# Optimization experiments

Measured on AMD Instinct MI355X. Metric: run time of the kernel, lower is better.

Reference implementation:

```python
import jax, jax.numpy as jnp
import numpy as np

D_MODEL = 512
N_HEADS = 16
D_HEAD = D_MODEL // N_HEADS


def _relative_shift(pos_score):
    # pos_score: [B, H, T, T]  (Transformer-XL shift trick)
    B, H, T1, T2 = pos_score.shape
    padded = jnp.pad(pos_score, ((0, 0), (0, 0), (0, 0), (1, 0)))  # [B,H,T1,T2+1]
    padded = padded.reshape(B, H, T2 + 1, T1)
    return padded[:, :, 1:].reshape(B, H, T1, T2)


def setup_inputs() -> dict:
    key = jax.random.key(0)
    ks = jax.random.split(key, 12)
    B, T, D = 4, 1024, D_MODEL
    s = 1.0 / np.sqrt(D)
    return {
        "q": jax.random.normal(ks[0], (B, T, D), jnp.float32),
        "k": jax.random.normal(ks[1], (B, T, D), jnp.float32),
        "v": jax.random.normal(ks[2], (B, T, D), jnp.float32),
        "pos_embedding": jax.random.normal(ks[3], (B, T, D), jnp.float32),
        "Wq": jax.random.normal(ks[4], (D, D), jnp.float32) * s,
        "bq": jnp.zeros((D,), jnp.float32),
        "Wp": jax.random.normal(ks[5], (D, D), jnp.float32) * s,
        "Wf": jax.random.normal(ks[6], (D, D), jnp.float32) * s,
        "bf": jnp.zeros((D,), jnp.float32),
        "u_bias": jax.random.normal(ks[7], (N_HEADS, D_HEAD), jnp.float32) * s,
        "v_bias": jax.random.normal(ks[8], (N_HEADS, D_HEAD), jnp.float32) * s,
    }


def reference(q, k, v, pos_embedding, Wq, bq, Wp, Wf, bf, u_bias, v_bias):
    B, T, D = q.shape
    H, Dh = N_HEADS, D_HEAD
    sqrt_dim = jnp.asarray(np.sqrt(D_MODEL), q.dtype)
    # NOTE: original module uses linear_q for q, k AND v (faithful to source)
    qh = (q @ Wq + bq).reshape(B, T, H, Dh)            # [B,T,H,Dh]
    kh = (k @ Wq + bq).reshape(B, T, H, Dh)
    vh = (v @ Wq + bq).reshape(B, T, H, Dh)
    ph = (pos_embedding @ Wp).reshape(B, T, H, Dh)     # no bias

    content_score = jnp.einsum('bthd,bshd->bhts', qh + u_bias, kh)
    pos_score = jnp.einsum('bthd,bshd->bhts', qh + v_bias, ph)
    pos_score = _relative_shift(pos_score)

    score = (content_score + pos_score) / sqrt_dim     # [B,H,T,T]
    attn = jax.nn.softmax(score, axis=-1)              # dropout identity in eval
    context = jnp.einsum('bhts,bshd->bthd', attn, vh).reshape(B, T, D)
    return context @ Wf + bf
```

## Files before the change

kernel.cpp:

```cpp
#include <hip/hip_runtime.h>
#include <hip/hip_bf16.h>

typedef __bf16 bf16;
typedef bf16 bf16x8 __attribute__((ext_vector_type(8)));
typedef bf16 bf16x4 __attribute__((ext_vector_type(4)));
typedef float f32x4 __attribute__((ext_vector_type(4)));
typedef _Float16 f16x4 __attribute__((ext_vector_type(4)));

#define SCALE_LOG2 0.06376237f


__global__ __launch_bounds__(256) void prep_kernel(
    const float* __restrict__ Wq, const float* __restrict__ Wp, const float* __restrict__ Wf,
    bf16* __restrict__ WqT, bf16* __restrict__ WpT, bf16* __restrict__ WfT)
{
  const int tid = threadIdx.x;
  __shared__ bf16 t[64][72];
  const int m = blockIdx.x >> 6;
  const int tb = blockIdx.x & 63;
  const int tr = tb >> 3, tc = tb & 7;
  const float* W = (m == 0) ? Wq : (m == 1) ? Wp : Wf;
  bf16*        O = (m == 0) ? WqT : (m == 1) ? WpT : WfT;
  const int r = tid >> 2, cg = tid & 3;
  {
    const float* src = W + (size_t)(tr * 64 + r) * 512 + tc * 64 + cg * 16;
    f32x4 a = *(const f32x4*)src, b2 = *(const f32x4*)(src + 4);
    f32x4 c = *(const f32x4*)(src + 8), d = *(const f32x4*)(src + 12);
    bf16x8 lo, hi;
#pragma unroll
    for (int j = 0; j < 4; j++) { lo[j] = (bf16)a[j]; lo[4 + j] = (bf16)b2[j]; hi[j] = (bf16)c[j]; hi[4 + j] = (bf16)d[j]; }
    *(bf16x8*)(&t[r][cg * 16])     = lo;
    *(bf16x8*)(&t[r][cg * 16 + 8]) = hi;
  }
  __syncthreads();
  bf16x8 o0, o1;
#pragma unroll
  for (int j = 0; j < 8; j++) { o0[j] = t[cg * 16 + j][r]; o1[j] = t[cg * 16 + 8 + j][r]; }
  bf16* dst = O + (size_t)(tc * 64 + r) * 512 + tr * 64 + cg * 16;
  *(bf16x8*)dst = o0;
  *(bf16x8*)(dst + 8) = o1;
}

__global__ __launch_bounds__(256) void proj_gemm(
    const float* __restrict__ q, const float* __restrict__ k, const float* __restrict__ v,
    const float* __restrict__ pos,
    const bf16* __restrict__ WqT, const bf16* __restrict__ WpT, const float* __restrict__ bq,
    bf16* __restrict__ qh, bf16* __restrict__ kh, bf16* __restrict__ vT, bf16* __restrict__ phx)
{
  __shared__ bf16 As[128 * 72];
  __shared__ bf16 Bs[128 * 72];
  const int tid = threadIdx.x;
  const int wave = tid >> 6, lane = tid & 63, quad = lane >> 4, ln = lane & 15;
  const int wg = blockIdx.x;
  const int xcd = wg & 7, sidx = wg >> 3;
  const int tn = sidx & 3;
  const int tm = xcd + ((sidx >> 2) << 3);
  const int kind = tm >> 5;
  const int rr0 = (tm & 31) * 128;
  const float* X = (kind == 0) ? q : (kind == 1) ? k : (kind == 2) ? v : pos;
  const bf16* WT = ((kind < 3) ? WqT : WpT) + (size_t)tn * 128 * 512;
  const int qn_ = (wave & 1) * 64;
  const int qr_ = (wave >> 1) * 64;
  const int srow = tid >> 2, scg = tid & 3;

  f32x4 acc[4][4] = {};

  for (int kk = 0; kk < 8; kk++) {
    const int k0 = kk * 64;
    {
      const float* p0 = X + (size_t)(rr0 + srow) * 512 + k0 + scg * 16;
      const float* p1 = X + (size_t)(rr0 + srow + 64) * 512 + k0 + scg * 16;
#pragma unroll
      for (int h = 0; h < 2; h++) {
        const float* p = h ? p1 : p0;
        f32x4 a = *(const f32x4*)p, b2 = *(const f32x4*)(p + 4);
        f32x4 c = *(const f32x4*)(p + 8), d = *(const f32x4*)(p + 12);
        bf16x8 lo, hi;
#pragma unroll
        for (int j = 0; j < 4; j++) { lo[j] = (bf16)a[j]; lo[4 + j] = (bf16)b2[j]; hi[j] = (bf16)c[j]; hi[4 + j] = (bf16)d[j]; }
        *(bf16x8*)(As + (srow + h * 64) * 72 + scg * 16)     = lo;
        *(bf16x8*)(As + (srow + h * 64) * 72 + scg * 16 + 8) = hi;
      }
      const bf16* w0 = WT + (size_t)srow * 512 + k0 + scg * 16;
      const bf16* w1 = WT + (size_t)(srow + 64) * 512 + k0 + scg * 16;
      *(bf16x8*)(Bs + srow * 72 + scg * 16)            = *(const bf16x8*)w0;
      *(bf16x8*)(Bs + srow * 72 + scg * 16 + 8)        = *(const bf16x8*)(w0 + 8);
      *(bf16x8*)(Bs + (srow + 64) * 72 + scg * 16)     = *(const bf16x8*)w1;
      *(bf16x8*)(Bs + (srow + 64) * 72 + scg * 16 + 8) = *(const bf16x8*)(w1 + 8);
    }
    __syncthreads();
#pragma unroll
    for (int ks = 0; ks < 2; ks++) {
      bf16x8 wf[4], xf[4];
#pragma unroll
      for (int i = 0; i < 4; i++) {
        wf[i] = *(const bf16x8*)(Bs + (qn_ + i * 16 + ln) * 72 + ks * 32 + quad * 8);
        xf[i] = *(const bf16x8*)(As + (qr_ + i * 16 + ln) * 72 + ks * 32 + quad * 8);
      }
#pragma unroll
      for (int i = 0; i < 4; i++)
#pragma unroll
        for (int j = 0; j < 4; j++)
          acc[i][j] = __builtin_amdgcn_mfma_f32_16x16x32_bf16(wf[i], xf[j], acc[i][j], 0, 0, 0);
    }
    __syncthreads();
  }

#pragma unroll
  for (int i = 0; i < 4; i++) {
    const int nn0 = tn * 128 + qn_ + i * 16 + quad * 4;
    const int dd0 = nn0 & 31, hh = nn0 >> 5;
    f32x4 b4 = {0.f, 0.f, 0.f, 0.f};
    if (kind < 3) b4 = *(const f32x4*)(bq + nn0);
#pragma unroll
    for (int j = 0; j < 4; j++) {
      const int rr = rr0 + qr_ + j * 16 + ln;
      const int bb = rr >> 10, tt = rr & 1023;
      const size_t base = (size_t)(bb * 16 + hh);
      bf16x4 pk;
#pragma unroll
      for (int r = 0; r < 4; r++) pk[r] = (bf16)(acc[i][j][r] + b4[r]);
      if (kind == 0)      *(bf16x4*)(qh + (base * 1024 + tt) * 32 + dd0) = pk;
      else if (kind == 1) *(bf16x4*)(kh + (base * 1024 + tt) * 32 + dd0) = pk;
      else if (kind == 2) {
#pragma unroll
        for (int r = 0; r < 4; r++) vT[(base * 32 + dd0 + r) * 1024 + tt] = pk[r];
      } else {
        *(bf16x4*)(phx + (base * 2048 + tt) * 32 + dd0) = pk;
        if (tt <= 1021) *(bf16x4*)(phx + (base * 2048 + tt + 1025) * 32 + dd0) = pk;
        if (tt == 1023) {
          bf16x4 zz = {};
          *(bf16x4*)(phx + (base * 2048 + 1024) * 32 + dd0) = zz;
          *(bf16x4*)(phx + (base * 2048 + 2047) * 32 + dd0) = zz;
        }
      }
    }
  }
}

__global__ __launch_bounds__(256, 4) void attn_kernel(
    const bf16* __restrict__ qh, const bf16* __restrict__ kh,
    const bf16* __restrict__ vT, const bf16* __restrict__ phx,
    const float* __restrict__ u_bias, const float* __restrict__ v_bias,
    float* __restrict__ Oa, float* __restrict__ Ob,
    float* __restrict__ la, float* __restrict__ lb)
{
  __shared__ bf16     kst[64 * 40];
  __shared__ bf16     phs[128 * 40];
  __shared__ bf16     vst[32 * 72];
  __shared__ _Float16 fs[4 * 16 * 84];
  __shared__ bf16     pb[4 * 16 * 72];

  const int tid = threadIdx.x;
  const int wave = tid >> 6, lane = tid & 63, quad = lane >> 4, ln = lane & 15;
  const int wg = blockIdx.x;
  const int bh = wg & 63;
  const int rest = wg >> 6;
  const int tq = rest & 15, sc = rest >> 4;
  const int h = bh & 15, b = bh >> 4;
  const int t0 = tq * 64;
  const bf16* qh_h  = qh  + (size_t)bh * 1024 * 32;
  const bf16* kh_h  = kh  + (size_t)bh * 1024 * 32;
  const bf16* vT_h  = vT  + (size_t)bh * 32 * 1024;
  const bf16* phx_h = phx + (size_t)bh * 2048 * 32;

  _Float16* fsw = fs + wave * 16 * 84;
  bf16*     pbw = pb + wave * 16 * 72;

  const int sr4 = tid >> 2, sc4 = tid & 3;
  const int sr8 = tid >> 3, sc8 = tid & 7;

  bf16x8 qu, qva, qvn;
  {
    const int t = t0 + wave * 16 + ln;
    bf16x8 q0 = *(const bf16x8*)(qh_h + (size_t)t * 32 + quad * 8);
    bf16x8 q1 = *(const bf16x8*)(qh_h + (size_t)(t + 1) * 32 + quad * 8);
    const float* ubp = u_bias + h * 32 + quad * 8;
    const float* vbp = v_bias + h * 32 + quad * 8;
#pragma unroll
    for (int j = 0; j < 8; j++) {
      qu[j]  = (bf16)(((float)q0[j] + ubp[j]) * SCALE_LOG2);
      qva[j] = (bf16)(((float)q0[j] + vbp[j]) * SCALE_LOG2);
      qvn[j] = (bf16)(((float)q1[j] + vbp[j]) * SCALE_LOG2);
    }
  }

  f32x4 O0 = {0.f, 0.f, 0.f, 0.f}, O1 = {0.f, 0.f, 0.f, 0.f};
  float l_lane = 0.0f;
  const f32x4 zf = {0.f, 0.f, 0.f, 0.f};

  const int si0 = sc * 8;

  bf16x8 g0, g1, g2, g3;
  {
    const int s0p = si0 * 64, jbp = s0p - t0 + 960;
    g0 = *(const bf16x8*)(kh_h  + (size_t)(s0p + sr4) * 32 + sc4 * 8);
    g1 = *(const bf16x8*)(phx_h + (size_t)(jbp + sr4) * 32 + sc4 * 8);
    g2 = *(const bf16x8*)(phx_h + (size_t)(jbp + 64 + sr4) * 32 + sc4 * 8);
    g3 = *(const bf16x8*)(vT_h  + (size_t)sr8 * 1024 + s0p + sc8 * 8);
  }

  for (int si = si0; si < si0 + 8; si++) {
    const int s0 = si * 64;
    const int jbase = s0 - t0 + 960;
    const int jb0 = jbase + (3 - wave) * 16;

    __syncthreads();

    *(bf16x8*)(kst + sr4 * 40 + sc4 * 8)        = g0;
    *(bf16x8*)(phs + sr4 * 40 + sc4 * 8)        = g1;
    *(bf16x8*)(phs + (64 + sr4) * 40 + sc4 * 8) = g2;
    *(bf16x8*)(vst + sr8 * 72 + sc8 * 8)        = g3;

    __syncthreads();

    if (si != si0 + 7) {
      const int s0n = s0 + 64, jbn = jbase + 64;
      g0 = *(const bf16x8*)(kh_h  + (size_t)(s0n + sr4) * 32 + sc4 * 8);
      g1 = *(const bf16x8*)(phx_h + (size_t)(jbn + sr4) * 32 + sc4 * 8);
      g2 = *(const bf16x8*)(phx_h + (size_t)(jbn + 64 + sr4) * 32 + sc4 * 8);
      g3 = *(const bf16x8*)(vT_h  + (size_t)sr8 * 1024 + s0n + sc8 * 8);
    }

#pragma unroll
    for (int i = 0; i < 5; i++) {
      const int row = (3 - wave + i) * 16 + ln;
      bf16x8 pbf = *(const bf16x8*)(phs + row * 40 + quad * 8);
      bf16x8 bsel = (jb0 + i * 16 >= 1024) ? qvn : qva;
      f32x4 f = __builtin_amdgcn_mfma_f32_16x16x32_bf16(pbf, bsel, zf, 0, 0, 0);
      f16x4 fh;
#pragma unroll
      for (int r = 0; r < 4; r++) fh[r] = (_Float16)f[r];
      *(f16x4*)(fsw + ln * 84 + i * 16 + quad * 4) = fh;
    }

    f32x4 c[4];
#pragma unroll
    for (int cs = 0; cs < 4; cs++) {
      bf16x8 kbf = *(const bf16x8*)(kst + (cs * 16 + ln) * 40 + quad * 8);
      c[cs] = __builtin_amdgcn_mfma_f32_16x16x32_bf16(kbf, qu, zf, 0, 0, 0);
    }

#pragma unroll
    for (int cs = 0; cs < 4; cs++) {
      bf16x4 pk;
#pragma unroll
      for (int r = 0; r < 4; r++) {
        const int col = cs * 16 + quad * 4 + r - ln + 15;
        const float p = __builtin_amdgcn_exp2f(c[cs][r] + (float)fsw[ln * 84 + col]);
        l_lane += p;
        pk[r] = (bf16)p;
      }
      *(bf16x4*)(pbw + ln * 72 + cs * 16 + quad * 4) = pk;
    }

#pragma unroll
    for (int kb = 0; kb < 2; kb++) {
      bf16x8 a  = *(const bf16x8*)(pbw + ln * 72 + kb * 32 + quad * 8);
      bf16x8 b0 = *(const bf16x8*)(vst + ln * 72 + kb * 32 + quad * 8);
      bf16x8 b1 = *(const bf16x8*)(vst + (16 + ln) * 72 + kb * 32 + quad * 8);
      O0 = __builtin_amdgcn_mfma_f32_16x16x32_bf16(a, b0, O0, 0, 0, 0);
      O1 = __builtin_amdgcn_mfma_f32_16x16x32_bf16(a, b1, O1, 0, 0, 0);
    }
  }

  l_lane += __shfl_xor(l_lane, 16);
  l_lane += __shfl_xor(l_lane, 32);

  float* Op = sc ? Ob : Oa;
  float* lp = sc ? lb : la;
#pragma unroll
  for (int r = 0; r < 4; r++) {
    const int t = t0 + wave * 16 + quad * 4 + r;
    const size_t o = ((size_t)(b * 1024 + t)) * 512 + h * 32;
    Op[o + ln]      = O0[r];
    Op[o + 16 + ln] = O1[r];
  }
  if (lane < 16) lp[(size_t)bh * 1024 + t0 + wave * 16 + lane] = l_lane;
}

__global__ __launch_bounds__(256) void out_gemm(
    const float* __restrict__ Oa, const float* __restrict__ Ob,
    const float* __restrict__ la, const float* __restrict__ lb,
    const bf16* __restrict__ WfT, const float* __restrict__ bfv,
    float* __restrict__ out)
{
  __shared__ bf16 As[64 * 40];
  __shared__ bf16 Bs[128 * 40];
  __shared__ float linv[16 * 64];
  const int tid = threadIdx.x;
  const int wave = tid >> 6, lane = tid & 63, quad = lane >> 4, ln = lane & 15;
  const int wg = blockIdx.x;
  const int xcd = wg & 7, sidx = wg >> 3;
  const int tn = sidx & 3;
  const int tm = xcd + ((sidx >> 2) << 3);
  const int rr0 = tm * 64;
  const bf16* WT = WfT + (size_t)tn * 128 * 512;
  const int qm = (wave & 1) * 32, qn = (wave >> 1) * 64;
  const int srow = tid >> 2, scg = tid & 3;

  for (int e = tid; e < 1024; e += 256) {
    const int hh = e >> 6, r = e & 63;
    const int row = rr0 + r;
    const int b_ = row >> 10, t_ = row & 1023;
    const size_t li = ((size_t)(b_ * 16 + hh)) * 1024 + t_;
    linv[e] = 1.0f / (la[li] + lb[li]);
  }
  __syncthreads();

  f32x4 acc[2][4] = {};
  for (int kk = 0; kk < 16; kk++) {
    const int k0 = kk * 32;
    {
      const float* pa = Oa + (size_t)(rr0 + srow) * 512 + k0 + scg * 8;
      const float* pcb = Ob + (size_t)(rr0 + srow) * 512 + k0 + scg * 8;
      f32x4 a0 = *(const f32x4*)pa,  a1 = *(const f32x4*)(pa + 4);
      f32x4 c0 = *(const f32x4*)pcb, c1 = *(const f32x4*)(pcb + 4);
      const float s = linv[kk * 64 + srow];
      bf16x8 t8;
#pragma unroll
      for (int j = 0; j < 4; j++) {
        t8[j]     = (bf16)((a0[j] + c0[j]) * s);
        t8[4 + j] = (bf16)((a1[j] + c1[j]) * s);
      }
      *(bf16x8*)(As + srow * 40 + scg * 8) = t8;
    }
    *(bf16x8*)(Bs + srow * 40 + scg * 8)        = *(const bf16x8*)(WT + (size_t)srow * 512 + k0 + scg * 8);
    *(bf16x8*)(Bs + (srow + 64) * 40 + scg * 8) = *(const bf16x8*)(WT + (size_t)(srow + 64) * 512 + k0 + scg * 8);
    __syncthreads();
    bf16x8 af[2], bfm[4];
#pragma unroll
    for (int i = 0; i < 2; i++)
      af[i] = *(const bf16x8*)(As + (qm + i * 16 + ln) * 40 + quad * 8);
#pragma unroll
    for (int j = 0; j < 4; j++)
      bfm[j] = *(const bf16x8*)(Bs + (qn + j * 16 + ln) * 40 + quad * 8);
#pragma unroll
    for (int i = 0; i < 2; i++)
#pragma unroll
      for (int j = 0; j < 4; j++)
        acc[i][j] = __builtin_amdgcn_mfma_f32_16x16x32_bf16(af[i], bfm[j], acc[i][j], 0, 0, 0);
    __syncthreads();
  }

#pragma unroll
  for (int i = 0; i < 2; i++)
#pragma unroll
    for (int j = 0; j < 4; j++) {
      const int nn = tn * 128 + qn + j * 16 + ln;
      const float bias = bfv[nn];
#pragma unroll
      for (int r = 0; r < 4; r++) {
        const int rr = rr0 + qm + i * 16 + quad * 4 + r;
        out[(size_t)rr * 512 + nn] = acc[i][j][r] + bias;
      }
    }
}

extern "C" void kernel_launch(void* const* d_in, const int* in_sizes, int n_in,
                              void* d_out, int out_size, void* d_ws, size_t ws_size,
                              hipStream_t stream) {
  const float* q   = (const float*)d_in[0];
  const float* k   = (const float*)d_in[1];
  const float* v   = (const float*)d_in[2];
  const float* pe  = (const float*)d_in[3];
  const float* Wq  = (const float*)d_in[4];
  const float* bq  = (const float*)d_in[5];
  const float* Wp  = (const float*)d_in[6];
  const float* Wf  = (const float*)d_in[7];
  const float* bfv = (const float*)d_in[8];
  const float* ub  = (const float*)d_in[9];
  const float* vb  = (const float*)d_in[10];

  bf16* ws  = (bf16*)d_ws;
  bf16* qh  = ws;
  bf16* kh  = qh + 2097152;
  bf16* vT  = kh + 2097152;
  bf16* phx = vT + 2097152;
  bf16* WqT = phx + 4194304;
  bf16* WpT = WqT + 262144;
  bf16* WfT = WpT + 262144;
  float* Oa = (float*)(WfT + 262144);
  float* Ob = Oa + 2097152;
  float* la = Ob + 2097152;
  float* lb = la + 65536;

  prep_kernel<<<192, 256, 0, stream>>>(Wq, Wp, Wf, WqT, WpT, WfT);
  proj_gemm<<<512, 256, 0, stream>>>(q, k, v, pe, WqT, WpT, bq, qh, kh, vT, phx);
  attn_kernel<<<2048, 256, 0, stream>>>(qh, kh, vT, phx, ub, vb, Oa, Ob, la, lb);
  out_gemm<<<256, 256, 0, stream>>>(Oa, Ob, la, lb, WfT, bfv, (float*)d_out);
}
```

Before: 183.5 us.

## Prefetch GEMM tiles into registers, stage V transpose via LDS, vectorize shift gather

In the projection and output GEMMs, the next K-slice of global data is now loaded into registers while the current slice is multiplied. This hides global load latency behind the MFMAs at the cost of more registers. The V projection epilogue now transposes through a padded LDS tile, so vT gets coalesced 16-byte stores instead of scattered 2-byte stores, which adds shared memory. In the attention kernel, the per-element relative-shift gather from LDS becomes two 64-bit loads plus a funnel shift.

After: 162.0 us. 11.7% less time.

```diff
diff --git a/kernel.cpp b/kernel.cpp
--- a/kernel.cpp
+++ b/kernel.cpp
@@ -49,6 +49,7 @@
 {
   __shared__ bf16 As[128 * 72];
   __shared__ bf16 Bs[128 * 72];
+  __shared__ bf16 vtile[128 * 132];
   const int tid = threadIdx.x;
   const int wave = tid >> 6, lane = tid & 63, quad = lane >> 4, ln = lane & 15;
   const int wg = blockIdx.x;
@@ -65,30 +66,52 @@
 
   f32x4 acc[4][4] = {};
 
+  f32x4  xa0[4], xa1[4];
+  bf16x8 wr0[2], wr1[2];
+  {
+    const float* p0 = X + (size_t)(rr0 + srow) * 512 + scg * 16;
+    const float* p1 = X + (size_t)(rr0 + srow + 64) * 512 + scg * 16;
+#pragma unroll
+    for (int u = 0; u < 4; u++) { xa0[u] = *(const f32x4*)(p0 + u * 4); xa1[u] = *(const f32x4*)(p1 + u * 4); }
+    const bf16* w0 = WT + (size_t)srow * 512 + scg * 16;
+    const bf16* w1 = WT + (size_t)(srow + 64) * 512 + scg * 16;
+    wr0[0] = *(const bf16x8*)w0; wr0[1] = *(const bf16x8*)(w0 + 8);
+    wr1[0] = *(const bf16x8*)w1; wr1[1] = *(const bf16x8*)(w1 + 8);
+  }
+
   for (int kk = 0; kk < 8; kk++) {
-    const int k0 = kk * 64;
+    __syncthreads();
     {
-      const float* p0 = X + (size_t)(rr0 + srow) * 512 + k0 + scg * 16;
-      const float* p1 = X + (size_t)(rr0 + srow + 64) * 512 + k0 + scg * 16;
-#pragma unroll
-      for (int h = 0; h < 2; h++) {
-        const float* p = h ? p1 : p0;
-        f32x4 a = *(const f32x4*)p, b2 = *(const f32x4*)(p + 4);
-        f32x4 c = *(const f32x4*)(p + 8), d = *(const f32x4*)(p + 12);
-        bf16x8 lo, hi;
-#pragma unroll
-        for (int j = 0; j < 4; j++) { lo[j] = (bf16)a[j]; lo[4 + j] = (bf16)b2[j]; hi[j] = (bf16)c[j]; hi[4 + j] = (bf16)d[j]; }
-        *(bf16x8*)(As + (srow + h * 64) * 72 + scg * 16)     = lo;
-        *(bf16x8*)(As + (srow + h * 64) * 72 + scg * 16 + 8) = hi;
-      }
-      const bf16* w0 = WT + (size_t)srow * 512 + k0 + scg * 16;
-      const bf16* w1 = WT + (size_t)(srow + 64) * 512 + k0 + scg * 16;
-      *(bf16x8*)(Bs + srow * 72 + scg * 16)            = *(const bf16x8*)w0;
-      *(bf16x8*)(Bs + srow * 72 + scg * 16 + 8)        = *(const bf16x8*)(w0 + 8);
-      *(bf16x8*)(Bs + (srow + 64) * 72 + scg * 16)     = *(const bf16x8*)w1;
-      *(bf16x8*)(Bs + (srow + 64) * 72 + scg * 16 + 8) = *(const bf16x8*)(w1 + 8);
-    }
-    __syncthreads();
+      bf16x8 lo, hi;
+#pragma unroll
+      for (int j = 0; j < 4; j++) { lo[j] = (bf16)xa0[j >> 2 ? 0 : 0][0], lo[j] = (bf16)xa0[0][j]; }
+#pragma unroll
+      for (int j = 0; j < 4; j++) { lo[j] = (bf16)xa0[0][j]; lo[4 + j] = (bf16)xa0[1][j]; hi[j] = (bf16)xa0[2][j]; hi[4 + j] = (bf16)xa0[3][j]; }
+      *(bf16x8*)(As + srow * 72 + scg * 16)     = lo;
+      *(bf16x8*)(As + srow * 72 + scg * 16 + 8) = hi;
+#pragma unroll
+      for (int j = 0; j < 4; j++) { lo[j] = (bf16)xa1[0][j]; lo[4 + j] = (bf16)xa1[1][j]; hi[j] = (bf16)xa1[2][j]; hi[4 + j] = (bf16)xa1[3][j]; }
+      *(bf16x8*)(As + (srow + 64) * 72 + scg * 16)     = lo;
+      *(bf16x8*)(As + (srow + 64) * 72 + scg * 16 + 8) = hi;
+      *(bf16x8*)(Bs + srow * 72 + scg * 16)            = wr0[0];
+      *(bf16x8*)(Bs + srow * 72 + scg * 16 + 8)        = wr0[1];
+      *(bf16x8*)(Bs + (srow + 64) * 72 + scg * 16)     = wr1[0];
+      *(bf16x8*)(Bs + (srow + 64) * 72 + scg * 16 + 8) = wr1[1];
+    }
+    __syncthreads();
+
+    if (kk < 7) {
+      const int k0n = (kk + 1) * 64;
+      const float* p0 = X + (size_t)(rr0 + srow) * 512 + k0n + scg * 16;
+      const float* p1 = X + (size_t)(rr0 + srow + 64) * 512 + k0n + scg * 16;
+#pragma unroll
+      for (int u = 0; u < 4; u++) { xa0[u] = *(const f32x4*)(p0 + u * 4); xa1[u] = *(const f32x4*)(p1 + u * 4); }
+      const bf16* w0 = WT + (size_t)srow * 512 + k0n + scg * 16;
+      const bf16* w1 = WT + (size_t)(srow + 64) * 512 + k0n + scg * 16;
+      wr0[0] = *(const bf16x8*)w0; wr0[1] = *(const bf16x8*)(w0 + 8);
+      wr1[0] = *(const bf16x8*)w1; wr1[1] = *(const bf16x8*)(w1 + 8);
+    }
+
 #pragma unroll
     for (int ks = 0; ks < 2; ks++) {
       bf16x8 wf[4], xf[4];
@@ -103,35 +126,59 @@
         for (int j = 0; j < 4; j++)
           acc[i][j] = __builtin_amdgcn_mfma_f32_16x16x32_bf16(wf[i], xf[j], acc[i][j], 0, 0, 0);
     }
-    __syncthreads();
-  }
-
-#pragma unroll
-  for (int i = 0; i < 4; i++) {
-    const int nn0 = tn * 128 + qn_ + i * 16 + quad * 4;
-    const int dd0 = nn0 & 31, hh = nn0 >> 5;
-    f32x4 b4 = {0.f, 0.f, 0.f, 0.f};
-    if (kind < 3) b4 = *(const f32x4*)(bq + nn0);
-#pragma unroll
-    for (int j = 0; j < 4; j++) {
-      const int rr = rr0 + qr_ + j * 16 + ln;
-      const int bb = rr >> 10, tt = rr & 1023;
-      const size_t base = (size_t)(bb * 16 + hh);
-      bf16x4 pk;
-#pragma unroll
-      for (int r = 0; r < 4; r++) pk[r] = (bf16)(acc[i][j][r] + b4[r]);
-      if (kind == 0)      *(bf16x4*)(qh + (base * 1024 + tt) * 32 + dd0) = pk;
-      else if (kind == 1) *(bf16x4*)(kh + (base * 1024 + tt) * 32 + dd0) = pk;
-      else if (kind == 2) {
-#pragma unroll
-        for (int r = 0; r < 4; r++) vT[(base * 32 + dd0 + r) * 1024 + tt] = pk[r];
-      } else {
-        *(bf16x4*)(phx + (base * 2048 + tt) * 32 + dd0) = pk;
-        if (tt <= 1021) *(bf16x4*)(phx + (base * 2048 + tt + 1025) * 32 + dd0) = pk;
-        if (tt == 1023) {
-          bf16x4 zz = {};
-          *(bf16x4*)(phx + (base * 2048 + 1024) * 32 + dd0) = zz;
-          *(bf16x4*)(phx + (base * 2048 + 2047) * 32 + dd0) = zz;
+  }
+  __syncthreads();
+
+  if (kind == 2) {
+#pragma unroll
+    for (int i = 0; i < 4; i++) {
+      const int nloc = qn_ + i * 16 + quad * 4;
+      f32x4 b4 = *(const f32x4*)(bq + tn * 128 + nloc);
+#pragma unroll
+      for (int j = 0; j < 4; j++) {
+        const int mloc = qr_ + j * 16 + ln;
+        bf16x4 pk;
+#pragma unroll
+        for (int r = 0; r < 4; r++) pk[r] = (bf16)(acc[i][j][r] + b4[r]);
+        *(bf16x4*)(vtile + mloc * 132 + nloc) = pk;
+      }
+    }
+    __syncthreads();
+    const int n = tid >> 1, mh = (tid & 1) * 64;
+    const int bb2 = rr0 >> 10, tt0 = rr0 & 1023;
+    bf16* vdst = vT + ((size_t)(bb2 * 16 + tn * 4 + (n >> 5)) * 32 + (n & 31)) * 1024 + tt0 + mh;
+#pragma unroll
+    for (int c = 0; c < 8; c++) {
+      bf16x8 oc;
+#pragma unroll
+      for (int e = 0; e < 8; e++) oc[e] = vtile[(mh + c * 8 + e) * 132 + n];
+      *(bf16x8*)(vdst + c * 8) = oc;
+    }
+  } else {
+#pragma unroll
+    for (int i = 0; i < 4; i++) {
+      const int nn0 = tn * 128 + qn_ + i * 16 + quad * 4;
+      const int dd0 = nn0 & 31, hh = nn0 >> 5;
+      f32x4 b4 = {0.f, 0.f, 0.f, 0.f};
+      if (kind < 3) b4 = *(const f32x4*)(bq + nn0);
+#pragma unroll
+      for (int j = 0; j < 4; j++) {
+        const int rr = rr0 + qr_ + j * 16 + ln;
+        const int bb = rr >> 10, tt = rr & 1023;
+        const size_t base = (size_t)(bb * 16 + hh);
+        bf16x4 pk;
+#pragma unroll
+        for (int r = 0; r < 4; r++) pk[r] = (bf16)(acc[i][j][r] + b4[r]);
+        if (kind == 0)      *(bf16x4*)(qh + (base * 1024 + tt) * 32 + dd0) = pk;
+        else if (kind == 1) *(bf16x4*)(kh + (base * 1024 + tt) * 32 + dd0) = pk;
+        else {
+          *(bf16x4*)(phx + (base * 2048 + tt) * 32 + dd0) = pk;
+          if (tt <= 1021) *(bf16x4*)(phx + (base * 2048 + tt + 1025) * 32 + dd0) = pk;
+          if (tt == 1023) {
+            bf16x4 zz = {};
+            *(bf16x4*)(phx + (base * 2048 + 1024) * 32 + dd0) = zz;
+            *(bf16x4*)(phx + (base * 2048 + 2047) * 32 + dd0) = zz;
+          }
         }
       }
     }
@@ -170,6 +217,9 @@
   const int sr4 = tid >> 2, sc4 = tid & 3;
   const int sr8 = tid >> 3, sc8 = tid & 7;
 
+  const int Ab  = quad * 4 + ((15 - ln) & ~3);
+  const int msh = ((15 - ln) & 3) * 16;
+
   bf16x8 qu, qva, qvn;
   {
     const int t = t0 + wave * 16 + ln;
@@ -241,13 +291,17 @@
       c[cs] = __builtin_amdgcn_mfma_f32_16x16x32_bf16(kbf, qu, zf, 0, 0, 0);
     }
 
+    const _Float16* rowp = fsw + ln * 84;
 #pragma unroll
     for (int cs = 0; cs < 4; cs++) {
+      const uint64_t v0 = *(const uint64_t*)(rowp + cs * 16 + Ab);
+      const uint64_t v1 = *(const uint64_t*)(rowp + cs * 16 + Ab + 4);
+      union { uint64_t u; f16x4 v; } W;
+      W.u = (v0 >> msh) | ((v1 << 1) << (63 - msh));
       bf16x4 pk;
 #pragma unroll
       for (int r = 0; r < 4; r++) {
-        const int col = cs * 16 + quad * 4 + r - ln + 15;
-        const float p = __builtin_amdgcn_exp2f(c[cs][r] + (float)fsw[ln * 84 + col]);
+        const float p = __builtin_amdgcn_exp2f(c[cs][r] + (float)W.v[r]);
         l_lane += p;
         pk[r] = (bf16)p;
       }
@@ -299,6 +353,17 @@
   const int qm = (wave & 1) * 32, qn = (wave >> 1) * 64;
   const int srow = tid >> 2, scg = tid & 3;
 
+  f32x4 a0, a1, c0, c1;
+  bf16x8 b0r, b1r;
+  {
+    const float* pa  = Oa + (size_t)(rr0 + srow) * 512 + scg * 8;
+    const float* pcb = Ob + (size_t)(rr0 + srow) * 512 + scg * 8;
+    a0 = *(const f32x4*)pa;  a1 = *(const f32x4*)(pa + 4);
+    c0 = *(const f32x4*)pcb; c1 = *(const f32x4*)(pcb + 4);
+    b0r = *(const bf16x8*)(WT + (size_t)srow * 512 + scg * 8);
+    b1r = *(const bf16x8*)(WT + (size_t)(srow + 64) * 512 + scg * 8);
+  }
+
   for (int e = tid; e < 1024; e += 256) {
     const int hh = e >> 6, r = e & 63;
     const int row = rr0 + r;
@@ -306,16 +371,11 @@
     const size_t li = ((size_t)(b_ * 16 + hh)) * 1024 + t_;
     linv[e] = 1.0f / (la[li] + lb[li]);
   }
-  __syncthreads();
 
   f32x4 acc[2][4] = {};
   for (int kk = 0; kk < 16; kk++) {
-    const int k0 = kk * 32;
+    __syncthreads();
     {
-      const float* pa = Oa + (size_t)(rr0 + srow) * 512 + k0 + scg * 8;
-      const float* pcb = Ob + (size_t)(rr0 + srow) * 512 + k0 + scg * 8;
-      f32x4 a0 = *(const f32x4*)pa,  a1 = *(const f32x4*)(pa + 4);
-      f32x4 c0 = *(const f32x4*)pcb, c1 = *(const f32x4*)(pcb + 4);
       const float s = linv[kk * 64 + srow];
       bf16x8 t8;
 #pragma unroll
@@ -323,11 +383,22 @@
         t8[j]     = (bf16)((a0[j] + c0[j]) * s);
         t8[4 + j] = (bf16)((a1[j] + c1[j]) * s);
       }
-      *(bf16x8*)(As + srow * 40 + scg * 8) = t8;
-    }
-    *(bf16x8*)(Bs + srow * 40 + scg * 8)        = *(const bf16x8*)(WT + (size_t)srow * 512 + k0 + scg * 8);
-    *(bf16x8*)(Bs + (srow + 64) * 40 + scg * 8) = *(const bf16x8*)(WT + (size_t)(srow + 64) * 512 + k0 + scg * 8);
-    __syncthreads();
+      *(bf16x8*)(As + srow * 40 + scg * 8)        = t8;
+      *(bf16x8*)(Bs + srow * 40 + scg * 8)        = b0r;
+      *(bf16x8*)(Bs + (srow + 64) * 40 + scg * 8) = b1r;
+    }
+    __syncthreads();
+
+    if (kk < 15) {
+      const int k0n = (kk + 1) * 32;
+      const float* pa  = Oa + (size_t)(rr0 + srow) * 512 + k0n + scg * 8;
+      const float* pcb = Ob + (size_t)(rr0 + srow) * 512 + k0n + scg * 8;
+      a0 = *(const f32x4*)pa;  a1 = *(const f32x4*)(pa + 4);
+      c0 = *(const f32x4*)pcb; c1 = *(const f32x4*)(pcb + 4);
+      b0r = *(const bf16x8*)(WT + (size_t)srow * 512 + k0n + scg * 8);
+      b1r = *(const bf16x8*)(WT + (size_t)(srow + 64) * 512 + k0n + scg * 8);
+    }
+
     bf16x8 af[2], bfm[4];
 #pragma unroll
     for (int i = 0; i < 2; i++)
@@ -340,7 +411,6 @@
 #pragma unroll
       for (int j = 0; j < 4; j++)
         acc[i][j] = __builtin_amdgcn_mfma_f32_16x16x32_bf16(af[i], bfm[j], acc[i][j], 0, 0, 0);
-    __syncthreads();
   }
 
 #pragma unroll
```
